# Kernel optimization log

Measured on AMD Instinct MI355X. Metric: run time of the kernel, lower is better.

The kernel has to match this reference:

```python
import jax, jax.numpy as jnp
import numpy as np

# ---- HashGrid config (tcnn defaults from module __init__) ----
N_LEVELS = 6
F = 2                      # n_features_per_level
T = 2 ** 19                # hashmap size
BASE = 16                  # base_resolution, per_level_scale=2.0
_RES = [BASE * (2 ** l) for l in range(N_LEVELS)]          # 16..512
_SIZES = [min(r ** 3, T) for r in _RES]                    # dense if grid fits
_OFFSETS = [0] + list(np.cumsum(_SIZES))
TOTAL_ENTRIES = int(_OFFSETS[-1])
_PRIMES = (1, 2654435761, 805459861)
BOX_R = 1.0
DIM_H = 64
DIM_IN = 3 + N_LEVELS * F


def hash_encode(xn, grid):
    """Multi-res hash-grid encoding. xn: [N,3] in [0,1]; grid: [TOTAL_ENTRIES, F]."""
    feats = []
    for l in range(N_LEVELS):
        res, size, off = _RES[l], _SIZES[l], _OFFSETS[l]
        dense = (res ** 3) <= T
        pos = xn * jnp.float32(res - 1) + 0.5          # tcnn: scale*x + 0.5
        pg = jnp.floor(pos)
        frac = pos - pg                                # [N,3]
        pgi = pg.astype(jnp.uint32)
        acc = jnp.zeros((xn.shape[0], F), xn.dtype)
        for corner in range(8):                        # trilinear, 8 corners
            cb = jnp.array([(corner >> d) & 1 for d in range(3)], dtype=jnp.uint32)
            c = pgi + cb                               # [N,3] corner coords
            w = jnp.prod(jnp.where(cb == 1, frac, 1.0 - frac), axis=-1)  # [N]
            if dense:
                c = jnp.minimum(c, jnp.uint32(res - 1))
                idx = c[:, 0] + c[:, 1] * jnp.uint32(res) + c[:, 2] * jnp.uint32(res * res)
            else:
                idx = ((c[:, 0] * jnp.uint32(_PRIMES[0]))
                       ^ (c[:, 1] * jnp.uint32(_PRIMES[1]))
                       ^ (c[:, 2] * jnp.uint32(_PRIMES[2]))) % jnp.uint32(size)
            acc = acc + w[:, None] * grid[jnp.uint32(off) + idx]
        feats.append(acc)
    return jnp.concatenate(feats, axis=-1)             # [N, 12]


def setup_inputs() -> dict:
    key = jax.random.key(0)
    k0, k1, k2 = jax.random.split(key, 3)
    N = 2_097_152
    x = jax.random.uniform(k0, (N, 3), jnp.float32, -1.0, 1.0)
    grid = jax.random.uniform(k1, (TOTAL_ENTRIES, F), jnp.float32, -1e-2, 1e-2)
    W0 = jax.random.normal(k2, (DIM_IN, DIM_H), jnp.float32) * float(np.sqrt(2.0 / DIM_H))
    b0 = jnp.zeros((DIM_H,), jnp.float32)
    W1 = jnp.full((DIM_H, 1), float(np.sqrt(np.pi / DIM_H)), jnp.float32)
    b1 = jnp.full((1,), -1.0, jnp.float32)             # -init_radius
    return {"x": x, "grid": grid, "W0": W0, "b0": b0, "W1": W1, "b1": b1}


def reference(x, grid, W0, b0, W1, b1):
    xn = (x + BOX_R) / (2.0 * BOX_R)                   # normalize to [0,1]
    f = hash_encode(xn, grid)                          # [N,12]
    h = jnp.concatenate([x, f], axis=-1)               # [N,15]
    h = jax.nn.relu(h @ W0 + b0)                       # [N,64]
    return h @ W1 + b1                                 # [N,1] scalar level s
```

## Files before the change

kernel.cpp:

```cpp
#include <hip/hip_runtime.h>


#define HP1 2654435761u
#define HP2 805459861u
#define HMASK ((1u << 19) - 1u)

typedef float v2f __attribute__((ext_vector_type(2)));

static __device__ __forceinline__ unsigned umin_(unsigned a, unsigned b) {
    return a < b ? a : b;
}

static __device__ __forceinline__ unsigned f2bf(float f) {
    unsigned u = __float_as_uint(f);
    return (u + 0x7fffu + ((u >> 16) & 1u)) >> 16;
}
static __device__ __forceinline__ float bf2f_lo(unsigned p) {
    return __uint_as_float((p & 0xffffu) << 16);
}
static __device__ __forceinline__ float bf2f_hi(unsigned p) {
    return __uint_as_float(p & 0xffff0000u);
}

static __device__ __forceinline__ v2f vmax0(v2f s) {
#if __has_builtin(__builtin_elementwise_max)
    return __builtin_elementwise_max(s, (v2f)0.0f);
#else
    v2f r; r.x = fmaxf(s.x, 0.0f); r.y = fmaxf(s.y, 0.0f); return r;
#endif
}

__global__ __launch_bounds__(256) void prep_kernel(
    const float* __restrict__ W0, const float* __restrict__ b0,
    const float* __restrict__ W1, const float* __restrict__ b1,
    const float2* __restrict__ gtab,
    float* __restrict__ wt, unsigned* __restrict__ packed)
{
    for (int t = blockIdx.x * 256 + threadIdx.x; t < 36864;
         t += gridDim.x * 256) {
        const float2 e = gtab[t];
        packed[t] = f2bf(e.x) | (f2bf(e.y) << 16);
    }
    if (blockIdx.x == 0) {
        for (int t = threadIdx.x; t < 1024; t += 256) {
            const int j = t >> 4, i = t & 15;
            wt[t] = (i == 15) ? b0[j] : W0[i * 64 + j];
        }
        if (threadIdx.x < 64) wt[1024 + threadIdx.x] = W1[threadIdx.x];
        if (threadIdx.x == 0) wt[1088] = b1[0];
    }
}

__global__ __launch_bounds__(256) void hash_level_kernel(
    const float* __restrict__ x,
    const float2* __restrict__ tab,
    unsigned* __restrict__ feat,
    float scale, int N)
{
    const int gid = blockIdx.x * 256 + threadIdx.x;
    if (gid >= N) return;

    const float px = __builtin_nontemporal_load(x + 3 * gid + 0);
    const float py = __builtin_nontemporal_load(x + 3 * gid + 1);
    const float pz = __builtin_nontemporal_load(x + 3 * gid + 2);

    const float p0 = fmaf((px + 1.0f) * 0.5f, scale, 0.5f);
    const float p1 = fmaf((py + 1.0f) * 0.5f, scale, 0.5f);
    const float p2 = fmaf((pz + 1.0f) * 0.5f, scale, 0.5f);
    const float g0 = floorf(p0), g1 = floorf(p1), g2 = floorf(p2);
    const float f0 = p0 - g0, f1 = p1 - g1, f2 = p2 - g2;
    const unsigned i0 = (unsigned)g0, i1 = (unsigned)g1, i2 = (unsigned)g2;

    const float wx[2] = {1.0f - f0, f0};
    const float wy[2] = {1.0f - f1, f1};
    const float wz[2] = {1.0f - f2, f2};
    const unsigned hx[2] = {i0, i0 + 1u};
    const unsigned hy[2] = {i1 * HP1, (i1 + 1u) * HP1};
    const unsigned hz[2] = {i2 * HP2, (i2 + 1u) * HP2};

    unsigned idx[8];
    float w[8];
    #pragma unroll
    for (int c = 0; c < 8; ++c) {
        const int bx = c & 1, by = (c >> 1) & 1, bz = (c >> 2) & 1;
        idx[c] = (hx[bx] ^ hy[by] ^ hz[bz]) & HMASK;
        w[c] = wx[bx] * wy[by] * wz[bz];
    }
    float2 v[8];
    #pragma unroll
    for (int c = 0; c < 8; ++c) v[c] = tab[idx[c]];

    float a0 = 0.0f, a1 = 0.0f;
    #pragma unroll
    for (int c = 0; c < 8; ++c) {
        a0 = fmaf(w[c], v[c].x, a0);
        a1 = fmaf(w[c], v[c].y, a1);
    }
    __builtin_nontemporal_store(f2bf(a0) | (f2bf(a1) << 16), feat + gid);
}

static __device__ __forceinline__ void dense_level(
    const float2* __restrict__ tab, unsigned res,
    float xn0, float xn1, float xn2, float& o0, float& o1)
{
    const float scale = (float)(res - 1);
    const float p0 = fmaf(xn0, scale, 0.5f);
    const float p1 = fmaf(xn1, scale, 0.5f);
    const float p2 = fmaf(xn2, scale, 0.5f);
    const float g0 = floorf(p0), g1 = floorf(p1), g2 = floorf(p2);
    const float f0 = p0 - g0, f1 = p1 - g1, f2 = p2 - g2;
    const unsigned i0 = (unsigned)g0, i1 = (unsigned)g1, i2 = (unsigned)g2;

    const unsigned rm1 = res - 1u;
    const unsigned cx[2] = {umin_(i0, rm1), umin_(i0 + 1u, rm1)};
    const unsigned cy[2] = {umin_(i1, rm1) * res, umin_(i1 + 1u, rm1) * res};
    const unsigned cz[2] = {umin_(i2, rm1) * res * res,
                            umin_(i2 + 1u, rm1) * res * res};
    const float wx[2] = {1.0f - f0, f0};
    const float wy[2] = {1.0f - f1, f1};
    const float wz[2] = {1.0f - f2, f2};

    float a0 = 0.0f, a1 = 0.0f;
    #pragma unroll
    for (int c = 0; c < 8; ++c) {
        const int bx = c & 1, by = (c >> 1) & 1, bz = (c >> 2) & 1;
        const unsigned idx = cx[bx] + cy[by] + cz[bz];
        const float w = wx[bx] * wy[by] * wz[bz];
        const float2 v = tab[idx];
        a0 = fmaf(w, v.x, a0);
        a1 = fmaf(w, v.y, a1);
    }
    o0 = a0;
    o1 = a1;
}

static __device__ __forceinline__ void dense_level_lds(
    const unsigned* __restrict__ sPk, unsigned off, unsigned res,
    float xn0, float xn1, float xn2, float& o0, float& o1)
{
    const float scale = (float)(res - 1);
    const float p0 = fmaf(xn0, scale, 0.5f);
    const float p1 = fmaf(xn1, scale, 0.5f);
    const float p2 = fmaf(xn2, scale, 0.5f);
    const float g0 = floorf(p0), g1 = floorf(p1), g2 = floorf(p2);
    const float f0 = p0 - g0, f1 = p1 - g1, f2 = p2 - g2;
    const unsigned i0 = (unsigned)g0, i1 = (unsigned)g1, i2 = (unsigned)g2;

    const unsigned rm1 = res - 1u;
    const unsigned cx[2] = {umin_(i0, rm1), umin_(i0 + 1u, rm1)};
    const unsigned cy[2] = {umin_(i1, rm1) * res, umin_(i1 + 1u, rm1) * res};
    const unsigned cz[2] = {umin_(i2, rm1) * res * res,
                            umin_(i2 + 1u, rm1) * res * res};
    const float wx[2] = {1.0f - f0, f0};
    const float wy[2] = {1.0f - f1, f1};
    const float wz[2] = {1.0f - f2, f2};

    float a0 = 0.0f, a1 = 0.0f;
    #pragma unroll
    for (int c = 0; c < 8; ++c) {
        const int bx = c & 1, by = (c >> 1) & 1, bz = (c >> 2) & 1;
        const unsigned p = sPk[off + cx[bx] + cy[by] + cz[bz]];
        const float w = wx[bx] * wy[by] * wz[bz];
        a0 = fmaf(w, bf2f_lo(p), a0);
        a1 = fmaf(w, bf2f_hi(p), a1);
    }
    o0 = a0;
    o1 = a1;
}

template<int BLOCK, bool L1LDS>
__global__ __launch_bounds__(BLOCK, 4) void dense_mlp_kernel(
    const float* __restrict__ x,
    const float* __restrict__ grid,
    const unsigned* __restrict__ feat,
    const float* __restrict__ wt,
    const unsigned* __restrict__ packed,
    float* __restrict__ out, int N)
{
    extern __shared__ unsigned sPk[];
    const int tid = threadIdx.x;

    const int nstage = L1LDS ? 36864 : 4096;
    for (int t = tid; t < nstage; t += BLOCK)
        sPk[t] = packed[t];
    __syncthreads();

    const int base = blockIdx.x * (BLOCK * 4) + tid;
    const float2* gtab = (const float2*)grid;

    v2f hp[2][16];

    #pragma unroll
    for (int k = 0; k < 4; ++k) {
        const int g = base + BLOCK * k;
        const int gs = (g < N) ? g : 0;
        const int p = k >> 1, lane = k & 1;

        const float px = __builtin_nontemporal_load(x + 3 * gs + 0);
        const float py = __builtin_nontemporal_load(x + 3 * gs + 1);
        const float pz = __builtin_nontemporal_load(x + 3 * gs + 2);
        const float xn0 = (px + 1.0f) * 0.5f;
        const float xn1 = (py + 1.0f) * 0.5f;
        const float xn2 = (pz + 1.0f) * 0.5f;

        hp[p][0][lane] = px; hp[p][1][lane] = py; hp[p][2][lane] = pz;
        hp[p][15][lane] = 1.0f;

        float t3, t4, t5, t6, t7, t8;
        dense_level_lds(sPk, 0u, 16u, xn0, xn1, xn2, t3, t4);
        if (L1LDS)
            dense_level_lds(sPk, 4096u, 32u, xn0, xn1, xn2, t5, t6);
        else
            dense_level(gtab + 4096u, 32u, xn0, xn1, xn2, t5, t6);
        dense_level(gtab + 36864u, 64u, xn0, xn1, xn2, t7, t8);
        hp[p][3][lane] = t3; hp[p][4][lane] = t4;
        hp[p][5][lane] = t5; hp[p][6][lane] = t6;
        hp[p][7][lane] = t7; hp[p][8][lane] = t8;

        #pragma unroll
        for (int l = 0; l < 3; ++l) {
            const unsigned pk = __builtin_nontemporal_load(
                feat + (size_t)l * N + gs);
            hp[p][9 + 2 * l][lane]  = bf2f_lo(pk);
            hp[p][10 + 2 * l][lane] = bf2f_hi(pk);
        }
    }

    const float b1v = wt[1088];
    v2f o2[2];
    o2[0] = (v2f)b1v; o2[1] = (v2f)b1v;

    #pragma unroll 4
    for (int j = 0; j < 64; ++j) {
        float r[16];
        #pragma unroll
        for (int i = 0; i < 16; ++i)
            r[i] = wt[j * 16 + i];
        const float w1j = wt[1024 + j];
        #pragma unroll
        for (int p = 0; p < 2; ++p) {
            v2f s = (v2f)0.0f;
            #pragma unroll
            for (int i = 0; i < 16; ++i)
                s = hp[p][i] * r[i] + s;
            s = vmax0(s);
            o2[p] = s * w1j + o2[p];
        }
    }

    #pragma unroll
    for (int k = 0; k < 4; ++k) {
        const int g = base + BLOCK * k;
        if (g < N)
            __builtin_nontemporal_store(o2[k >> 1][k & 1], out + g);
    }
}

extern "C" void kernel_launch(void* const* d_in, const int* in_sizes, int n_in,
                              void* d_out, int out_size, void* d_ws, size_t ws_size,
                              hipStream_t stream) {
    const float* x    = (const float*)d_in[0];
    const float* grid = (const float*)d_in[1];
    const float* W0   = (const float*)d_in[2];
    const float* b0   = (const float*)d_in[3];
    const float* W1   = (const float*)d_in[4];
    const float* b1   = (const float*)d_in[5];
    float* out = (float*)d_out;

    const int N = in_sizes[0] / 3;
    const int blocks1 = (N + 255) / 256;

    const float2* gtab = (const float2*)grid;

    auto align256 = [](size_t v) { return (v + 255) & ~(size_t)255; };
    size_t off = 0;
    const size_t feat_off = off; off += align256((size_t)3 * N * 4);
    const size_t wt_off   = off; off += align256(1089 * 4);
    const size_t pk_off   = off; off += align256(36864 * 4);
    (void)ws_size;

    unsigned* feat   = (unsigned*)((char*)d_ws + feat_off);
    float*    wt     = (float*)((char*)d_ws + wt_off);
    unsigned* packed = (unsigned*)((char*)d_ws + pk_off);

    prep_kernel<<<64, 256, 0, stream>>>(W0, b0, W1, b1, gtab, wt, packed);

    hash_level_kernel<<<blocks1, 256, 0, stream>>>(x, gtab + 299008u,
                                                   feat + (size_t)0 * N, 127.0f, N);
    hash_level_kernel<<<blocks1, 256, 0, stream>>>(x, gtab + 823296u,
                                                   feat + (size_t)1 * N, 255.0f, N);
    hash_level_kernel<<<blocks1, 256, 0, stream>>>(x, gtab + 1347584u,
                                                   feat + (size_t)2 * N, 511.0f, N);

    const size_t bigShm = 36864u * 4u;
    const void* bigK =
        reinterpret_cast<const void*>(&dense_mlp_kernel<1024, true>);
    (void)hipFuncSetAttribute(bigK,
        hipFuncAttributeMaxDynamicSharedMemorySize, (int)bigShm);
    bool big = false;
    hipFuncAttributes fa{};
    if (hipFuncGetAttributes(&fa, bigK) == hipSuccess)
        big = ((size_t)fa.maxDynamicSharedSizeBytes >= bigShm);

    if (big) {
        const int blocksB = (N + 4095) / 4096;
        dense_mlp_kernel<1024, true><<<blocksB, 1024, bigShm, stream>>>(
            x, (const float*)grid, feat, wt, packed, out, N);
    } else {
        const int blocksF = (N + 1023) / 1024;
        dense_mlp_kernel<256, false><<<blocksF, 256, 4096u * 4u, stream>>>(
            x, (const float*)grid, feat, wt, packed, out, N);
    }
}
```

Before: 318.6 us.

## Merge prep into first hash launch and prefetch level-2 gathers before LDS work

New measurement: 318.4 us. About the same (-0.1%).

```diff
diff --git a/kernel.cpp b/kernel.cpp
--- a/kernel.cpp
+++ b/kernel.cpp
@@ -30,34 +30,11 @@
 #endif
 }
 
-__global__ __launch_bounds__(256) void prep_kernel(
-    const float* __restrict__ W0, const float* __restrict__ b0,
-    const float* __restrict__ W1, const float* __restrict__ b1,
-    const float2* __restrict__ gtab,
-    float* __restrict__ wt, unsigned* __restrict__ packed)
-{
-    for (int t = blockIdx.x * 256 + threadIdx.x; t < 36864;
-         t += gridDim.x * 256) {
-        const float2 e = gtab[t];
-        packed[t] = f2bf(e.x) | (f2bf(e.y) << 16);
-    }
-    if (blockIdx.x == 0) {
-        for (int t = threadIdx.x; t < 1024; t += 256) {
-            const int j = t >> 4, i = t & 15;
-            wt[t] = (i == 15) ? b0[j] : W0[i * 64 + j];
-        }
-        if (threadIdx.x < 64) wt[1024 + threadIdx.x] = W1[threadIdx.x];
-        if (threadIdx.x == 0) wt[1088] = b1[0];
-    }
-}
-
-__global__ __launch_bounds__(256) void hash_level_kernel(
-    const float* __restrict__ x,
-    const float2* __restrict__ tab,
-    unsigned* __restrict__ feat,
-    float scale, int N)
-{
-    const int gid = blockIdx.x * 256 + threadIdx.x;
+static __device__ __forceinline__ void hash_body(
+    const float* __restrict__ x, const float2* __restrict__ tab,
+    unsigned* __restrict__ feat, float scale, int N, int bid)
+{
+    const int gid = bid * 256 + threadIdx.x;
     if (gid >= N) return;
 
     const float px = __builtin_nontemporal_load(x + 3 * gid + 0);
@@ -99,9 +76,43 @@
     __builtin_nontemporal_store(f2bf(a0) | (f2bf(a1) << 16), feat + gid);
 }
 
-static __device__ __forceinline__ void dense_level(
-    const float2* __restrict__ tab, unsigned res,
-    float xn0, float xn1, float xn2, float& o0, float& o1)
+__global__ __launch_bounds__(256) void hash3_prep_kernel(
+    const float* __restrict__ x, const float2* __restrict__ gtab,
+    unsigned* __restrict__ feat0, int N,
+    float* __restrict__ wt, unsigned* __restrict__ packed,
+    const float* __restrict__ W0, const float* __restrict__ b0,
+    const float* __restrict__ W1, const float* __restrict__ b1)
+{
+    const int nh = (int)gridDim.x - 64;
+    if ((int)blockIdx.x >= nh) {
+        const int pb = (int)blockIdx.x - nh;
+        for (int t = pb * 256 + threadIdx.x; t < 36864; t += 64 * 256) {
+            const float2 e = gtab[t];
+            packed[t] = f2bf(e.x) | (f2bf(e.y) << 16);
+        }
+        if (pb == 0) {
+            for (int t = threadIdx.x; t < 1024; t += 256) {
+                const int j = t >> 4, i = t & 15;
+                wt[t] = (i == 15) ? b0[j] : W0[i * 64 + j];
+            }
+            if (threadIdx.x < 64) wt[1024 + threadIdx.x] = W1[threadIdx.x];
+            if (threadIdx.x == 0) wt[1088] = b1[0];
+        }
+        return;
+    }
+    hash_body(x, gtab + 299008u, feat0, 127.0f, N, (int)blockIdx.x);
+}
+
+__global__ __launch_bounds__(256) void hash_level_kernel(
+    const float* __restrict__ x, const float2* __restrict__ tab,
+    unsigned* __restrict__ feat, float scale, int N)
+{
+    hash_body(x, tab, feat, scale, N, (int)blockIdx.x);
+}
+
+static __device__ __forceinline__ v2f lds_lerp(
+    const unsigned* __restrict__ sPk, unsigned off, unsigned res,
+    float xn0, float xn1, float xn2)
 {
     const float scale = (float)(res - 1);
     const float p0 = fmaf(xn0, scale, 0.5f);
@@ -120,23 +131,22 @@
     const float wy[2] = {1.0f - f1, f1};
     const float wz[2] = {1.0f - f2, f2};
 
-    float a0 = 0.0f, a1 = 0.0f;
+    v2f acc = (v2f)0.0f;
     #pragma unroll
     for (int c = 0; c < 8; ++c) {
         const int bx = c & 1, by = (c >> 1) & 1, bz = (c >> 2) & 1;
-        const unsigned idx = cx[bx] + cy[by] + cz[bz];
-        const float w = wx[bx] * wy[by] * wz[bz];
-        const float2 v = tab[idx];
-        a0 = fmaf(w, v.x, a0);
-        a1 = fmaf(w, v.y, a1);
-    }
-    o0 = a0;
-    o1 = a1;
-}
-
-static __device__ __forceinline__ void dense_level_lds(
-    const unsigned* __restrict__ sPk, unsigned off, unsigned res,
-    float xn0, float xn1, float xn2, float& o0, float& o1)
+        const unsigned q = sPk[off + cx[bx] + cy[by] + cz[bz]];
+        v2f uv;
+        uv.x = __uint_as_float(q << 16);
+        uv.y = __uint_as_float(q & 0xffff0000u);
+        acc = uv * (wx[bx] * wy[by] * wz[bz]) + acc;
+    }
+    return acc;
+}
+
+static __device__ __forceinline__ v2f global_lerp(
+    const float2* __restrict__ tab, unsigned res,
+    float xn0, float xn1, float xn2)
 {
     const float scale = (float)(res - 1);
     const float p0 = fmaf(xn0, scale, 0.5f);
@@ -155,17 +165,15 @@
     const float wy[2] = {1.0f - f1, f1};
     const float wz[2] = {1.0f - f2, f2};
 
-    float a0 = 0.0f, a1 = 0.0f;
+    v2f acc = (v2f)0.0f;
     #pragma unroll
     for (int c = 0; c < 8; ++c) {
         const int bx = c & 1, by = (c >> 1) & 1, bz = (c >> 2) & 1;
-        const unsigned p = sPk[off + cx[bx] + cy[by] + cz[bz]];
-        const float w = wx[bx] * wy[by] * wz[bz];
-        a0 = fmaf(w, bf2f_lo(p), a0);
-        a1 = fmaf(w, bf2f_hi(p), a1);
-    }
-    o0 = a0;
-    o1 = a1;
+        const float2 v = tab[cx[bx] + cy[by] + cz[bz]];
+        v2f uv; uv.x = v.x; uv.y = v.y;
+        acc = uv * (wx[bx] * wy[by] * wz[bz]) + acc;
+    }
+    return acc;
 }
 
 template<int BLOCK, bool L1LDS>
@@ -187,42 +195,92 @@
 
     const int base = blockIdx.x * (BLOCK * 4) + tid;
     const float2* gtab = (const float2*)grid;
+    const float2* tab2 = gtab + 36864u;
 
     v2f hp[2][16];
 
     #pragma unroll
-    for (int k = 0; k < 4; ++k) {
-        const int g = base + BLOCK * k;
-        const int gs = (g < N) ? g : 0;
-        const int p = k >> 1, lane = k & 1;
-
-        const float px = __builtin_nontemporal_load(x + 3 * gs + 0);
-        const float py = __builtin_nontemporal_load(x + 3 * gs + 1);
-        const float pz = __builtin_nontemporal_load(x + 3 * gs + 2);
-        const float xn0 = (px + 1.0f) * 0.5f;
-        const float xn1 = (py + 1.0f) * 0.5f;
-        const float xn2 = (pz + 1.0f) * 0.5f;
-
-        hp[p][0][lane] = px; hp[p][1][lane] = py; hp[p][2][lane] = pz;
-        hp[p][15][lane] = 1.0f;
-
-        float t3, t4, t5, t6, t7, t8;
-        dense_level_lds(sPk, 0u, 16u, xn0, xn1, xn2, t3, t4);
-        if (L1LDS)
-            dense_level_lds(sPk, 4096u, 32u, xn0, xn1, xn2, t5, t6);
-        else
-            dense_level(gtab + 4096u, 32u, xn0, xn1, xn2, t5, t6);
-        dense_level(gtab + 36864u, 64u, xn0, xn1, xn2, t7, t8);
-        hp[p][3][lane] = t3; hp[p][4][lane] = t4;
-        hp[p][5][lane] = t5; hp[p][6][lane] = t6;
-        hp[p][7][lane] = t7; hp[p][8][lane] = t8;
-
-        #pragma unroll
-        for (int l = 0; l < 3; ++l) {
-            const unsigned pk = __builtin_nontemporal_load(
-                feat + (size_t)l * N + gs);
-            hp[p][9 + 2 * l][lane]  = bf2f_lo(pk);
-            hp[p][10 + 2 * l][lane] = bf2f_hi(pk);
+    for (int p = 0; p < 2; ++p) {
+        float  xn[2][3];
+        float  fr[2][3];
+        float2 vg[2][8];
+        unsigned fw[2][3];
+
+        #pragma unroll
+        for (int e = 0; e < 2; ++e) {
+            const int k = 2 * p + e;
+            const int g = base + BLOCK * k;
+            const int gs = (g < N) ? g : 0;
+
+            const float px = __builtin_nontemporal_load(x + 3 * gs + 0);
+            const float py = __builtin_nontemporal_load(x + 3 * gs + 1);
+            const float pz = __builtin_nontemporal_load(x + 3 * gs + 2);
+            hp[p][0][e] = px; hp[p][1][e] = py; hp[p][2][e] = pz;
+            hp[p][15][e] = 1.0f;
+            xn[e][0] = (px + 1.0f) * 0.5f;
+            xn[e][1] = (py + 1.0f) * 0.5f;
+            xn[e][2] = (pz + 1.0f) * 0.5f;
+
+            const float q0 = fmaf(xn[e][0], 63.0f, 0.5f);
+            const float q1 = fmaf(xn[e][1], 63.0f, 0.5f);
+            const float q2 = fmaf(xn[e][2], 63.0f, 0.5f);
+            const float g0 = floorf(q0), g1 = floorf(q1), g2 = floorf(q2);
+            fr[e][0] = q0 - g0; fr[e][1] = q1 - g1; fr[e][2] = q2 - g2;
+            const unsigned i0 = (unsigned)g0, i1 = (unsigned)g1,
+                           i2 = (unsigned)g2;
+            const unsigned cx[2] = {umin_(i0, 63u), umin_(i0 + 1u, 63u)};
+            const unsigned cy[2] = {umin_(i1, 63u) * 64u,
+                                    umin_(i1 + 1u, 63u) * 64u};
+            const unsigned cz[2] = {umin_(i2, 63u) * 4096u,
+                                    umin_(i2 + 1u, 63u) * 4096u};
+            #pragma unroll
+            for (int c = 0; c < 8; ++c) {
+                const int bx = c & 1, by = (c >> 1) & 1, bz = (c >> 2) & 1;
+                vg[e][c] = tab2[cx[bx] + cy[by] + cz[bz]];
+            }
+            #pragma unroll
+            for (int l = 0; l < 3; ++l)
+                fw[e][l] = __builtin_nontemporal_load(
+                    feat + (size_t)l * N + gs);
+        }
+
+        #pragma unroll
+        for (int e = 0; e < 2; ++e) {
+            const v2f l0 = lds_lerp(sPk, 0u, 16u,
+                                    xn[e][0], xn[e][1], xn[e][2]);
+            hp[p][3][e] = l0.x; hp[p][4][e] = l0.y;
+            v2f l1;
+            if (L1LDS)
+                l1 = lds_lerp(sPk, 4096u, 32u,
+                              xn[e][0], xn[e][1], xn[e][2]);
+            else
+                l1 = global_lerp(gtab + 4096u, 32u,
+                                 xn[e][0], xn[e][1], xn[e][2]);
+            hp[p][5][e] = l1.x; hp[p][6][e] = l1.y;
+        }
+
+        #pragma unroll
+        for (int e = 0; e < 2; ++e) {
+            const float wx[2] = {1.0f - fr[e][0], fr[e][0]};
+            const float wy[2] = {1.0f - fr[e][1], fr[e][1]};
+            const float wz[2] = {1.0f - fr[e][2], fr[e][2]};
+            float wyz[4];
+            #pragma unroll
+            for (int c = 0; c < 4; ++c)
+                wyz[c] = wy[c & 1] * wz[c >> 1];
+            v2f acc = (v2f)0.0f;
+            #pragma unroll
+            for (int c = 0; c < 8; ++c) {
+                v2f uv; uv.x = vg[e][c].x; uv.y = vg[e][c].y;
+                acc = uv * (wx[c & 1] * wyz[c >> 1]) + acc;
+            }
+            hp[p][7][e] = acc.x; hp[p][8][e] = acc.y;
+
+            #pragma unroll
+            for (int l = 0; l < 3; ++l) {
+                hp[p][9 + 2 * l][e]  = bf2f_lo(fw[e][l]);
+                hp[p][10 + 2 * l][e] = bf2f_hi(fw[e][l]);
+            }
         }
     }
 
@@ -283,10 +341,8 @@
     float*    wt     = (float*)((char*)d_ws + wt_off);
     unsigned* packed = (unsigned*)((char*)d_ws + pk_off);
 
-    prep_kernel<<<64, 256, 0, stream>>>(W0, b0, W1, b1, gtab, wt, packed);
-
-    hash_level_kernel<<<blocks1, 256, 0, stream>>>(x, gtab + 299008u,
-                                                   feat + (size_t)0 * N, 127.0f, N);
+    hash3_prep_kernel<<<blocks1 + 64, 256, 0, stream>>>(
+        x, gtab, feat + (size_t)0 * N, N, wt, packed, W0, b0, W1, b1);
     hash_level_kernel<<<blocks1, 256, 0, stream>>>(x, gtab + 823296u,
                                                    feat + (size_t)1 * N, 255.0f, N);
     hash_level_kernel<<<blocks1, 256, 0, stream>>>(x, gtab + 1347584u,
```
